# Optimization experiments

Measured on AMD Instinct MI355X. Metric: run time of the kernel, lower is better.

## Reference

```python
import jax, jax.numpy as jnp
import numpy as np

H = 4096          # hidden_size
NH = 32           # num query heads
NKV = 8           # num kv heads
HD = H // NH      # head_dim = 128
NE = 8            # num_experts
TOPK = 2
ROPE_THETA = 10000.0
EPS = 1e-6


def rmsnorm(x, w):
    var = jnp.mean(x * x, axis=-1, keepdims=True)
    return x * jax.lax.rsqrt(var + EPS) * w


def apply_rope_neox(x, positions):
    # x: [N, heads, HD]; neox style: rotate halves
    half = HD // 2
    inv_freq = 1.0 / (ROPE_THETA ** (jnp.arange(0, HD, 2, dtype=jnp.float32) / HD))  # [half]
    ang = positions.astype(jnp.float32)[:, None] * inv_freq[None, :]                 # [N, half]
    cos = jnp.cos(ang)[:, None, :]  # [N,1,half]
    sin = jnp.sin(ang)[:, None, :]
    x1, x2 = x[..., :half], x[..., half:]
    return jnp.concatenate([x1 * cos - x2 * sin, x2 * cos + x1 * sin], axis=-1)


def setup_inputs() -> dict:
    key = jax.random.key(0)
    ks = jax.random.split(key, 6)
    N = 2048
    return {
        "positions": jnp.arange(N, dtype=jnp.int32),
        "hidden_states": jax.random.normal(ks[0], (N, H), dtype=jnp.float32),
        "w_qkv": jax.random.normal(ks[1], (H, (NH + 2 * NKV) * HD), dtype=jnp.float32) * 0.02,
        "w_o": jax.random.normal(ks[2], (NH * HD, H), dtype=jnp.float32) * 0.02,
        "w_gate": jax.random.normal(ks[3], (H, NE), dtype=jnp.float32) * 0.02,
        "rms_w_pre": jnp.ones((H,), dtype=jnp.float32),
        "rms_w_post": jnp.ones((H,), dtype=jnp.float32),
        "expert_logits": jax.random.uniform(ks[4], (N, NE), dtype=jnp.float32),
    }


def reference(positions, hidden_states, w_qkv, w_o, w_gate, rms_w_pre, rms_w_post, expert_logits):
    N = hidden_states.shape[0]
    # pre-attention RMSNorm (residual is None branch)
    residual = hidden_states
    x = rmsnorm(hidden_states, rms_w_pre)

    qkv = x @ w_qkv
    q = qkv[:, : NH * HD].reshape(N, NH, HD)
    k = qkv[:, NH * HD : (NH + NKV) * HD].reshape(N, NKV, HD)
    v = qkv[:, (NH + NKV) * HD :].reshape(N, NKV, HD)

    q = apply_rope_neox(q, positions)
    k = apply_rope_neox(k, positions)

    # GQA causal self-attention (prefill, single sequence)
    group = NH // NKV
    k_rep = jnp.repeat(k, group, axis=1)  # [N, NH, HD]
    v_rep = jnp.repeat(v, group, axis=1)
    scale = HD ** -0.5
    scores = jnp.einsum("qhd,khd->hqk", q, k_rep) * scale  # [NH, N, N]
    causal = jnp.tril(jnp.ones((N, N), dtype=bool))
    scores = jnp.where(causal[None], scores, jnp.finfo(scores.dtype).min)
    probs = jax.nn.softmax(scores, axis=-1)
    attn_out = jnp.einsum("hqk,khd->qhd", probs, v_rep).reshape(N, NH * HD)

    output = attn_out @ w_o
    # post-attention RMSNorm with fused residual add (vLLM semantics)
    s = output + residual
    residual = s
    output = rmsnorm(s, rms_w_post)

    router_logits = output @ w_gate  # computed as in source; routing result overwritten below

    # random_routing: topk over random expert logits, renormalized
    topk_weights, topk_ids = jax.lax.top_k(expert_logits, TOPK)  # [N, TOPK]
    topk_weights = topk_weights / jnp.sum(topk_weights, axis=-1, keepdims=True)

    # permute_by_exp_ids: stable sort of flattened expert ids, gather tokens
    reorder_ids = jnp.argsort(topk_ids.reshape(-1), stable=True)  # [N*TOPK]
    permuted_output = output[reorder_ids // TOPK]                 # [N*TOPK, H]
    return permuted_output, topk_weights, topk_ids, reorder_ids
```

## Files before the change

### kernel.cpp

```cpp
#include <hip/hip_runtime.h>
#include <hip/hip_bf16.h>
#include <math.h>

#define N_TOK 2048
#define H_DIM 4096
#define NH 32
#define NKV 8
#define HD 128
#define QKV_D 6144
#define NE 8
#define TOPK 2

#define OUT_PERM 0
#define OUT_W    16777216
#define OUT_IDS  16781312
#define OUT_REO  16785408

typedef __bf16 bf16x8 __attribute__((ext_vector_type(8)));
typedef float f32x4 __attribute__((ext_vector_type(4)));

typedef __attribute__((address_space(3))) void lds_void;
typedef __attribute__((address_space(1))) const void gbl_void;

__device__ __forceinline__ void gld16(const void* g, void* l) {
    __builtin_amdgcn_global_load_lds((gbl_void*)g, (lds_void*)l, 16, 0, 0);
}

__device__ __forceinline__ unsigned short f2bf(float f) {
    union { float f; unsigned u; } v; v.f = f;
    unsigned r = v.u + 0x7fff + ((v.u >> 16) & 1);
    return (unsigned short)(r >> 16);
}
__device__ __forceinline__ unsigned pack2bf(float a, float b) {
    return (unsigned)f2bf(a) | ((unsigned)f2bf(b) << 16);
}
__device__ __forceinline__ float bf2f(unsigned short u) {
    union { unsigned u; float f; } v; v.u = ((unsigned)u) << 16;
    return v.f;
}

__global__ __launch_bounds__(256) void rmsnorm_k(const float* __restrict__ x,
                                                 const float* __restrict__ w,
                                                 float* __restrict__ yf,
                                                 unsigned short* __restrict__ yb) {
    int row = blockIdx.x;
    int tid = threadIdx.x;
    const float4* x4 = (const float4*)(x + (size_t)row * H_DIM);
    const float4* w4 = (const float4*)w;
    float4 v[4];
    float ss = 0.f;
#pragma unroll
    for (int k = 0; k < 4; ++k) {
        v[k] = x4[tid + k * 256];
        ss += v[k].x * v[k].x + v[k].y * v[k].y + v[k].z * v[k].z + v[k].w * v[k].w;
    }
#pragma unroll
    for (int off = 32; off; off >>= 1) ss += __shfl_xor(ss, off);
    __shared__ float sacc[4];
    if ((tid & 63) == 0) sacc[tid >> 6] = ss;
    __syncthreads();
    float tot = sacc[0] + sacc[1] + sacc[2] + sacc[3];
    float sc = rsqrtf(tot * (1.0f / H_DIM) + 1e-6f);
#pragma unroll
    for (int k = 0; k < 4; ++k) {
        float4 ww = w4[tid + k * 256];
        float4 o;
        o.x = v[k].x * sc * ww.x;
        o.y = v[k].y * sc * ww.y;
        o.z = v[k].z * sc * ww.z;
        o.w = v[k].w * sc * ww.w;
        if (yf) {
            *(float4*)(yf + (size_t)row * H_DIM + (tid + k * 256) * 4) = o;
        } else {
            uint2 p;
            p.x = pack2bf(o.x, o.y);
            p.y = pack2bf(o.z, o.w);
            *(uint2*)(yb + (size_t)row * H_DIM + (tid + k * 256) * 4) = p;
        }
    }
}

__global__ __launch_bounds__(256) void convT_k(const float* __restrict__ src,
                                               unsigned short* __restrict__ dst,
                                               int R, int C) {
    __shared__ float t[64][68];
    int r0 = blockIdx.y * 64, c0 = blockIdx.x * 64;
    int tid = threadIdx.x;
    int lr = tid >> 4, lc = tid & 15;
#pragma unroll
    for (int it = 0; it < 4; ++it) {
        int r = lr + it * 16;
        float4 v = *(const float4*)(src + (size_t)(r0 + r) * C + c0 + lc * 4);
        *(float4*)&t[r][lc * 4] = v;
    }
    __syncthreads();
#pragma unroll
    for (int it = 0; it < 4; ++it) {
        int cc = lr + it * 16;
        uint2 o;
        o.x = pack2bf(t[lc * 4 + 0][cc], t[lc * 4 + 1][cc]);
        o.y = pack2bf(t[lc * 4 + 2][cc], t[lc * 4 + 3][cc]);
        *(uint2*)(dst + (size_t)(c0 + cc) * R + r0 + lc * 4) = o;
    }
}

__global__ __launch_bounds__(256) void gemm_k(const __hip_bfloat16* __restrict__ A,
                                              const __hip_bfloat16* __restrict__ Bt,
                                              float* __restrict__ C,
                                              unsigned short* __restrict__ Cb,
                                              const float* __restrict__ residual,
                                              int Ncols) {
    __shared__ __align__(16) __hip_bfloat16 As[128 * 64];
    __shared__ __align__(16) __hip_bfloat16 Bs[128 * 64];
    const int K = H_DIM;
    int tid = threadIdx.x, w = tid >> 6, lane = tid & 63;
    int quad = lane >> 4, l15 = lane & 15;
    int m0 = blockIdx.x * 128, n0 = blockIdx.y * 128;
    int wm = (w & 1) * 64, wn = (w >> 1) * 64;

    int rowInChunk = lane >> 3;
    int uIdx = lane & 7;
    const char* Ag[4]; const char* Bg[4];
    char* Al[4]; char* Bl[4];
#pragma unroll
    for (int c = 0; c < 4; ++c) {
        int ch = w * 4 + c;
        int r = ch * 8 + rowInChunk;
        int gu = uIdx ^ (r & 7);
        Ag[c] = (const char*)(A + (size_t)(m0 + r) * K) + gu * 16;
        Bg[c] = (const char*)(Bt + (size_t)(n0 + r) * K) + gu * 16;
        Al[c] = (char*)As + ch * 1024;
        Bl[c] = (char*)Bs + ch * 1024;
    }

    f32x4 acc[4][4];
#pragma unroll
    for (int i = 0; i < 4; ++i)
#pragma unroll
        for (int j = 0; j < 4; ++j) acc[i][j] = (f32x4){0.f, 0.f, 0.f, 0.f};

    for (int k0 = 0; k0 < K; k0 += 64) {
        __syncthreads();
#pragma unroll
        for (int c = 0; c < 4; ++c) gld16(Ag[c] + (size_t)k0 * 2, Al[c]);
#pragma unroll
        for (int c = 0; c < 4; ++c) gld16(Bg[c] + (size_t)k0 * 2, Bl[c]);
        __syncthreads();
#pragma unroll
        for (int kk = 0; kk < 2; ++kk) {
            bf16x8 af[4], bfr[4];
#pragma unroll
            for (int mt = 0; mt < 4; ++mt) {
                int m = wm + mt * 16 + l15;
                af[mt] = *(const bf16x8*)((const char*)As + m * 128 + (((kk * 4 + quad) ^ (m & 7)) * 16));
            }
#pragma unroll
            for (int nt = 0; nt < 4; ++nt) {
                int n = wn + nt * 16 + l15;
                bfr[nt] = *(const bf16x8*)((const char*)Bs + n * 128 + (((kk * 4 + quad) ^ (n & 7)) * 16));
            }
#pragma unroll
            for (int mt = 0; mt < 4; ++mt)
#pragma unroll
                for (int nt = 0; nt < 4; ++nt)
                    acc[mt][nt] = __builtin_amdgcn_mfma_f32_16x16x32_bf16(af[mt], bfr[nt], acc[mt][nt], 0, 0, 0);
        }
    }
#pragma unroll
    for (int mt = 0; mt < 4; ++mt)
#pragma unroll
        for (int nt = 0; nt < 4; ++nt)
#pragma unroll
            for (int r = 0; r < 4; ++r) {
                int row = m0 + wm + mt * 16 + quad * 4 + r;
                int col = n0 + wn + nt * 16 + l15;
                size_t off = (size_t)row * Ncols + col;
                float v = acc[mt][nt][r];
                if (Cb) {
                    Cb[off] = f2bf(v);
                } else {
                    if (residual) v += residual[off];
                    C[off] = v;
                }
            }
}

__global__ __launch_bounds__(256) void prep_k(const unsigned short* __restrict__ qkvb,
                                              const int* __restrict__ pos,
                                              unsigned short* __restrict__ Qc,
                                              unsigned short* __restrict__ Kc) {
    int row = blockIdx.x, tid = threadIdx.x;
    float fpos = (float)pos[row];
    const float scale = 0.08838834764831845f;
    const float lg = 0.20762050593045f;
#pragma unroll
    for (int it = 0; it < 8; ++it) {
        int pi = tid + it * 256;
        int head = pi >> 6, t = pi & 63;
        float inv = exp2f(-(float)t * lg);
        float ang = fpos * inv;
        float s = __sinf(ang), c = __cosf(ang);
        const unsigned short* bp = qkvb + (size_t)row * QKV_D + head * HD + t;
        float x1 = bf2f(bp[0]), x2 = bf2f(bp[64]);
        unsigned short* qb = Qc + (size_t)row * H_DIM + head * HD + t;
        qb[0]  = f2bf((x1 * c - x2 * s) * scale);
        qb[64] = f2bf((x2 * c + x1 * s) * scale);
    }
#pragma unroll
    for (int it = 0; it < 2; ++it) {
        int pi = tid + it * 256;
        int kvh = pi >> 6, t = pi & 63;
        float inv = exp2f(-(float)t * lg);
        float ang = fpos * inv;
        float s = __sinf(ang), c = __cosf(ang);
        const unsigned short* bp = qkvb + (size_t)row * QKV_D + H_DIM + kvh * HD + t;
        float x1 = bf2f(bp[0]), x2 = bf2f(bp[64]);
        unsigned short* kb = Kc + ((size_t)kvh * N_TOK + row) * HD + t;
        kb[0]  = f2bf(x1 * c - x2 * s);
        kb[64] = f2bf(x2 * c + x1 * s);
    }
}

__global__ __launch_bounds__(256) void vt_k(const unsigned short* __restrict__ qkvb,
                                            unsigned short* __restrict__ Vt) {
    __shared__ unsigned short ts[64][136];
    int j0 = blockIdx.x * 64, kvh = blockIdx.y, tid = threadIdx.x;
#pragma unroll
    for (int it = 0; it < 4; ++it) {
        int idx = tid + it * 256;
        int r = idx >> 4, c8 = idx & 15;
        *(uint4*)&ts[r][c8 * 8] =
            *(const uint4*)(qkvb + (size_t)(j0 + r) * QKV_D + (NH + NKV) * HD + kvh * HD + c8 * 8);
    }
    __syncthreads();
    int d = tid >> 1, half = tid & 1;
    unsigned short* dst = Vt + ((size_t)kvh * HD + d) * N_TOK + j0 + half * 32;
#pragma unroll
    for (int g = 0; g < 4; ++g) {
        int kb = half * 32 + g * 8;
        uint4 o;
        o.x = (unsigned)ts[kb + 0][d] | ((unsigned)ts[kb + 1][d] << 16);
        o.y = (unsigned)ts[kb + 2][d] | ((unsigned)ts[kb + 3][d] << 16);
        o.z = (unsigned)ts[kb + 4][d] | ((unsigned)ts[kb + 5][d] << 16);
        o.w = (unsigned)ts[kb + 6][d] | ((unsigned)ts[kb + 7][d] << 16);
        *(uint4*)(dst + g * 8) = o;
    }
}

__global__ __launch_bounds__(512) void attn_k(const __hip_bfloat16* __restrict__ Qc,
                                              const __hip_bfloat16* __restrict__ Kc,
                                              const __hip_bfloat16* __restrict__ Vt,
                                              unsigned short* __restrict__ ao) {
    __shared__ __align__(16) __hip_bfloat16 Ks[2][32 * 128];
    __shared__ __align__(16) __hip_bfloat16 Vs[2][128 * 32];
    __shared__ __align__(16) unsigned short Pw[8][16 * 40];

    int tid = threadIdx.x, w = tid >> 6, lane = tid & 63;
    int quad = lane >> 4, l15 = lane & 15;
    int pr = blockIdx.y;
    int kvh = pr >> 1;
    int h = kvh * 4 + (pr & 1) * 2 + (w & 1);
    int qt = gridDim.x - 1 - blockIdx.x;
    int i0 = qt * 64;
    int i0q = i0 + (w >> 1) * 16;
    int q = i0q + l15;

    bf16x8 qf[4];
    const __hip_bfloat16* qrow = Qc + (size_t)q * H_DIM + h * HD;
#pragma unroll
    for (int kf = 0; kf < 4; ++kf)
        qf[kf] = *(const bf16x8*)(qrow + kf * 32 + quad * 8);

    const char* KcH = (const char*)(Kc + (size_t)kvh * N_TOK * HD);
    const char* VtH = (const char*)(Vt + (size_t)kvh * HD * N_TOK);

    int kKey = w * 4 + (lane >> 4);
    int kPart = (lane & 15) ^ (kKey & 15);
    int vD = w * 16 + (lane >> 2);
    int vP = (lane & 3) ^ (vD & 3);
    char* Kl[2] = { (char*)&Ks[0][0] + w * 1024, (char*)&Ks[1][0] + w * 1024 };
    char* Vl[2] = { (char*)&Vs[0][0] + w * 1024, (char*)&Vs[1][0] + w * 1024 };

    float mstat = -INFINITY, lstat = 0.f;
    f32x4 o[8];
#pragma unroll
    for (int nt = 0; nt < 8; ++nt) o[nt] = (f32x4){0.f, 0.f, 0.f, 0.f};

    int nsteps = (i0 + 64) >> 5;

    gld16(KcH + (size_t)kKey * 256 + kPart * 16, Kl[0]);
    gld16(VtH + (size_t)vD * (N_TOK * 2) + vP * 16, Vl[0]);
    __syncthreads();

    for (int t = 0; t < nsteps; ++t) {
        int j0 = t << 5;
        int cur = t & 1;
        if (t + 1 < nsteps) {
            int jn = j0 + 32;
            gld16(KcH + (size_t)(jn + kKey) * 256 + kPart * 16, Kl[cur ^ 1]);
            gld16(VtH + (size_t)vD * (N_TOK * 2) + (size_t)jn * 2 + vP * 16, Vl[cur ^ 1]);
        }
        if (j0 <= i0q + 15) {
            const char* Kb = (const char*)&Ks[cur][0];
            const char* Vb = (const char*)&Vs[cur][0];

            f32x4 s[2];
            s[0] = (f32x4){0.f, 0.f, 0.f, 0.f};
            s[1] = (f32x4){0.f, 0.f, 0.f, 0.f};
#pragma unroll
            for (int mt = 0; mt < 2; ++mt) {
                int key = mt * 16 + l15;
#pragma unroll
                for (int kf = 0; kf < 4; ++kf) {
                    bf16x8 kfr = *(const bf16x8*)(Kb + key * 256 + (((kf * 4 + quad) ^ (key & 15)) * 16));
                    s[mt] = __builtin_amdgcn_mfma_f32_16x16x32_bf16(kfr, qf[kf], s[mt], 0, 0, 0);
                }
            }
            if (j0 + 31 > i0q) {
#pragma unroll
                for (int mt = 0; mt < 2; ++mt) {
                    int keyb = j0 + mt * 16 + quad * 4;
#pragma unroll
                    for (int r = 0; r < 4; ++r)
                        if (keyb + r > q) s[mt][r] = -INFINITY;
                }
            }
            float mx = fmaxf(fmaxf(fmaxf(s[0][0], s[0][1]), fmaxf(s[0][2], s[0][3])),
                             fmaxf(fmaxf(s[1][0], s[1][1]), fmaxf(s[1][2], s[1][3])));
            mx = fmaxf(mx, __shfl_xor(mx, 16));
            mx = fmaxf(mx, __shfl_xor(mx, 32));
            float newm = fmaxf(mstat, mx);
            float alpha = __expf(mstat - newm);
            float p[8];
#pragma unroll
            for (int mt = 0; mt < 2; ++mt)
#pragma unroll
                for (int r = 0; r < 4; ++r) p[mt * 4 + r] = __expf(s[mt][r] - newm);
            float ps = p[0] + p[1] + p[2] + p[3] + p[4] + p[5] + p[6] + p[7];
            ps += __shfl_xor(ps, 16);
            ps += __shfl_xor(ps, 32);
            lstat = lstat * alpha + ps;
            mstat = newm;

            unsigned* pwb = (unsigned*)(&Pw[w][0]);
            int eo = l15 * 20 + quad * 2;
            pwb[eo]     = pack2bf(p[0], p[1]);
            pwb[eo + 1] = pack2bf(p[2], p[3]);
            pwb[eo + 8] = pack2bf(p[4], p[5]);
            pwb[eo + 9] = pack2bf(p[6], p[7]);
            bf16x8 pf = *(const bf16x8*)(&Pw[w][l15 * 40 + quad * 8]);

            float alq[4];
#pragma unroll
            for (int r = 0; r < 4; ++r) alq[r] = __shfl(alpha, quad * 4 + r);
#pragma unroll
            for (int nt = 0; nt < 8; ++nt)
#pragma unroll
                for (int r = 0; r < 4; ++r) o[nt][r] *= alq[r];

#pragma unroll
            for (int nt = 0; nt < 8; ++nt) {
                int d = nt * 16 + l15;
                bf16x8 vf = *(const bf16x8*)(Vb + d * 64 + ((quad ^ (d & 3)) * 16));
                o[nt] = __builtin_amdgcn_mfma_f32_16x16x32_bf16(pf, vf, o[nt], 0, 0, 0);
            }
        }
        __syncthreads();
    }

    float linv[4];
#pragma unroll
    for (int r = 0; r < 4; ++r) linv[r] = 1.f / __shfl(lstat, quad * 4 + r);
#pragma unroll
    for (int nt = 0; nt < 8; ++nt)
#pragma unroll
        for (int r = 0; r < 4; ++r) {
            int row = i0q + quad * 4 + r;
            int col = h * HD + nt * 16 + l15;
            ao[(size_t)row * H_DIM + col] = f2bf(o[nt][r] * linv[r]);
        }
}

__global__ __launch_bounds__(256) void topk_k(const float* __restrict__ elog,
                                              float* __restrict__ w_out,
                                              float* __restrict__ id_out,
                                              int* __restrict__ ids_int) {
    int row = blockIdx.x * 256 + threadIdx.x;
    if (row >= N_TOK) return;
    const float4* e4 = (const float4*)(elog + (size_t)row * NE);
    float4 a = e4[0], b = e4[1];
    float e[8] = {a.x, a.y, a.z, a.w, b.x, b.y, b.z, b.w};
    int id0 = 0;
    float b0 = e[0];
#pragma unroll
    for (int t = 1; t < 8; ++t)
        if (e[t] > b0) { b0 = e[t]; id0 = t; }
    int id1 = -1;
    float b1 = -INFINITY;
#pragma unroll
    for (int t = 0; t < 8; ++t)
        if (t != id0 && e[t] > b1) { b1 = e[t]; id1 = t; }
    float s = b0 + b1;
    w_out[row * 2 + 0] = b0 / s;
    w_out[row * 2 + 1] = b1 / s;
    id_out[row * 2 + 0] = (float)id0;
    id_out[row * 2 + 1] = (float)id1;
    ids_int[row * 2 + 0] = id0;
    ids_int[row * 2 + 1] = id1;
}

__global__ __launch_bounds__(256) void sort_k(const int* __restrict__ ids,
                                              float* __restrict__ reorder_out,
                                              int* __restrict__ perm) {
    __shared__ int sh[N_TOK * TOPK];
    int tid = threadIdx.x;
    for (int r = tid; r < N_TOK * TOPK; r += 256) sh[r] = ids[r];
    __syncthreads();
    int i = blockIdx.x * 256 + tid;
    int e = sh[i];
    int rank = 0;
    for (int j = 0; j < N_TOK * TOPK; ++j) {
        int ej = sh[j];
        rank += (ej < e) ? 1 : ((ej == e && j < i) ? 1 : 0);
    }
    reorder_out[rank] = (float)i;
    perm[rank] = i;
}

__global__ __launch_bounds__(256) void gather_k(const float* __restrict__ src,
                                                const int* __restrict__ perm,
                                                float* __restrict__ dst) {
    int r = blockIdx.x;
    int srow = perm[r] >> 1;
    const float4* s4 = (const float4*)(src + (size_t)srow * H_DIM);
    float4* d4 = (float4*)(dst + (size_t)r * H_DIM);
    int tid = threadIdx.x;
#pragma unroll
    for (int k = 0; k < 4; ++k) d4[tid + k * 256] = s4[tid + k * 256];
}

extern "C" void kernel_launch(void* const* d_in, const int* in_sizes, int n_in,
                              void* d_out, int out_size, void* d_ws, size_t ws_size,
                              hipStream_t stream) {
    const int*   positions = (const int*)d_in[0];
    const float* hidden    = (const float*)d_in[1];
    const float* w_qkv     = (const float*)d_in[2];
    const float* w_o       = (const float*)d_in[3];
    const float* rms_pre   = (const float*)d_in[5];
    const float* rms_post  = (const float*)d_in[6];
    const float* elog      = (const float*)d_in[7];
    float* out = (float*)d_out;

    char* ws = (char*)d_ws;
    unsigned short* wqkvT = (unsigned short*)(ws);
    unsigned short* woT   = (unsigned short*)(ws);
    float*          post  = (float*)(ws + 33554432ULL);
    unsigned short* xn    = (unsigned short*)(ws + 50331648ULL);
    unsigned short* aout  = (unsigned short*)(ws + 50331648ULL);
    unsigned short* qkvb  = (unsigned short*)(ws + 67108864ULL);
    float*          sbuf  = (float*)(ws + 67108864ULL);
    unsigned short* Qc    = (unsigned short*)(ws + 117440512ULL);
    unsigned short* Kc    = (unsigned short*)(ws + 134217728ULL);
    unsigned short* Vt    = (unsigned short*)(ws + 138412032ULL);
    int* ids_int  = (int*)(ws + 142606336ULL);
    int* perm_int = (int*)(ws + 142622720ULL);

    convT_k<<<dim3(QKV_D / 64, H_DIM / 64), 256, 0, stream>>>(w_qkv, wqkvT, H_DIM, QKV_D);
    rmsnorm_k<<<N_TOK, 256, 0, stream>>>(hidden, rms_pre, nullptr, xn);
    gemm_k<<<dim3(N_TOK / 128, QKV_D / 128), 256, 0, stream>>>(
        (const __hip_bfloat16*)xn, (const __hip_bfloat16*)wqkvT, nullptr, qkvb, nullptr, QKV_D);
    convT_k<<<dim3(H_DIM / 64, H_DIM / 64), 256, 0, stream>>>(w_o, woT, H_DIM, H_DIM);
    prep_k<<<N_TOK, 256, 0, stream>>>(qkvb, positions, Qc, Kc);
    vt_k<<<dim3(N_TOK / 64, NKV), 256, 0, stream>>>(qkvb, Vt);
    attn_k<<<dim3(N_TOK / 64, 16), 512, 0, stream>>>(
        (const __hip_bfloat16*)Qc, (const __hip_bfloat16*)Kc, (const __hip_bfloat16*)Vt, aout);
    gemm_k<<<dim3(N_TOK / 128, H_DIM / 128), 256, 0, stream>>>(
        (const __hip_bfloat16*)aout, (const __hip_bfloat16*)woT, sbuf, nullptr, hidden, H_DIM);
    rmsnorm_k<<<N_TOK, 256, 0, stream>>>(sbuf, rms_post, post, nullptr);
    topk_k<<<N_TOK / 256, 256, 0, stream>>>(elog, out + OUT_W, out + OUT_IDS, ids_int);
    sort_k<<<(N_TOK * TOPK) / 256, 256, 0, stream>>>(ids_int, out + OUT_REO, perm_int);
    gather_k<<<N_TOK * TOPK, 256, 0, stream>>>(post, perm_int, out + OUT_PERM);
}
```

Before: 768.2 us.

## Double-buffer GEMM LDS tiles and remap workgroups across XCDs

Converts the GEMM main loop to a double-buffered LDS scheme that prefetches the next K tile while computing on the current one, with a single barrier per step. It also remaps the linear block index so consecutive workgroups, which share tiles, land on the same XCD for better L2 reuse. This doubles LDS usage per block, which may reduce occupancy.

```diff
diff --git a/kernel.cpp b/kernel.cpp
--- a/kernel.cpp
+++ b/kernel.cpp
@@ -110,18 +110,23 @@
                                               unsigned short* __restrict__ Cb,
                                               const float* __restrict__ residual,
                                               int Ncols) {
-    __shared__ __align__(16) __hip_bfloat16 As[128 * 64];
-    __shared__ __align__(16) __hip_bfloat16 Bs[128 * 64];
+    __shared__ __align__(16) __hip_bfloat16 As[2][128 * 64];
+    __shared__ __align__(16) __hip_bfloat16 Bs[2][128 * 64];
     const int K = H_DIM;
     int tid = threadIdx.x, w = tid >> 6, lane = tid & 63;
     int quad = lane >> 4, l15 = lane & 15;
-    int m0 = blockIdx.x * 128, n0 = blockIdx.y * 128;
+
+    int gx = gridDim.x;
+    int nwg = gx * gridDim.y;
+    int v = blockIdx.y * gx + blockIdx.x;
+    int lin = (v & 7) * (nwg >> 3) + (v >> 3);
+    int m0 = (lin % gx) * 128, n0 = (lin / gx) * 128;
     int wm = (w & 1) * 64, wn = (w >> 1) * 64;
 
     int rowInChunk = lane >> 3;
     int uIdx = lane & 7;
     const char* Ag[4]; const char* Bg[4];
-    char* Al[4]; char* Bl[4];
+    int chOff[4];
 #pragma unroll
     for (int c = 0; c < 4; ++c) {
         int ch = w * 4 + c;
@@ -129,8 +134,7 @@
         int gu = uIdx ^ (r & 7);
         Ag[c] = (const char*)(A + (size_t)(m0 + r) * K) + gu * 16;
         Bg[c] = (const char*)(Bt + (size_t)(n0 + r) * K) + gu * 16;
-        Al[c] = (char*)As + ch * 1024;
-        Bl[c] = (char*)Bs + ch * 1024;
+        chOff[c] = ch * 1024;
     }
 
     f32x4 acc[4][4];
@@ -139,25 +143,39 @@
 #pragma unroll
         for (int j = 0; j < 4; ++j) acc[i][j] = (f32x4){0.f, 0.f, 0.f, 0.f};
 
-    for (int k0 = 0; k0 < K; k0 += 64) {
-        __syncthreads();
-#pragma unroll
-        for (int c = 0; c < 4; ++c) gld16(Ag[c] + (size_t)k0 * 2, Al[c]);
-#pragma unroll
-        for (int c = 0; c < 4; ++c) gld16(Bg[c] + (size_t)k0 * 2, Bl[c]);
-        __syncthreads();
+    const int nsteps = K / 64;
+
+#pragma unroll
+    for (int c = 0; c < 4; ++c) gld16(Ag[c], (char*)&As[0][0] + chOff[c]);
+#pragma unroll
+    for (int c = 0; c < 4; ++c) gld16(Bg[c], (char*)&Bs[0][0] + chOff[c]);
+    __syncthreads();
+
+    for (int t = 0; t < nsteps; ++t) {
+        int cur = t & 1;
+        if (t + 1 < nsteps) {
+            size_t kb = (size_t)(t + 1) * 128;
+            char* dA = (char*)&As[cur ^ 1][0];
+            char* dB = (char*)&Bs[cur ^ 1][0];
+#pragma unroll
+            for (int c = 0; c < 4; ++c) gld16(Ag[c] + kb, dA + chOff[c]);
+#pragma unroll
+            for (int c = 0; c < 4; ++c) gld16(Bg[c] + kb, dB + chOff[c]);
+        }
+        const char* sA = (const char*)&As[cur][0];
+        const char* sB = (const char*)&Bs[cur][0];
 #pragma unroll
         for (int kk = 0; kk < 2; ++kk) {
             bf16x8 af[4], bfr[4];
 #pragma unroll
             for (int mt = 0; mt < 4; ++mt) {
                 int m = wm + mt * 16 + l15;
-                af[mt] = *(const bf16x8*)((const char*)As + m * 128 + (((kk * 4 + quad) ^ (m & 7)) * 16));
+                af[mt] = *(const bf16x8*)(sA + m * 128 + (((kk * 4 + quad) ^ (m & 7)) * 16));
             }
 #pragma unroll
             for (int nt = 0; nt < 4; ++nt) {
                 int n = wn + nt * 16 + l15;
-                bfr[nt] = *(const bf16x8*)((const char*)Bs + n * 128 + (((kk * 4 + quad) ^ (n & 7)) * 16));
+                bfr[nt] = *(const bf16x8*)(sB + n * 128 + (((kk * 4 + quad) ^ (n & 7)) * 16));
             }
 #pragma unroll
             for (int mt = 0; mt < 4; ++mt)
@@ -165,6 +183,7 @@
                 for (int nt = 0; nt < 4; ++nt)
                     acc[mt][nt] = __builtin_amdgcn_mfma_f32_16x16x32_bf16(af[mt], bfr[nt], acc[mt][nt], 0, 0, 0);
         }
+        __syncthreads();
     }
 #pragma unroll
     for (int mt = 0; mt < 4; ++mt)
@@ -175,12 +194,12 @@
                 int row = m0 + wm + mt * 16 + quad * 4 + r;
                 int col = n0 + wn + nt * 16 + l15;
                 size_t off = (size_t)row * Ncols + col;
-                float v = acc[mt][nt][r];
+                float vv = acc[mt][nt][r];
                 if (Cb) {
-                    Cb[off] = f2bf(v);
+                    Cb[off] = f2bf(vv);
                 } else {
-                    if (residual) v += residual[off];
-                    C[off] = v;
+                    if (residual) vv += residual[off];
+                    C[off] = vv;
                 }
             }
 }
```

After: 809.4 us. 1.05x slower.
